# Kernel tuning notes

Measured on AMD Instinct MI355X. Metric: run time of the kernel, lower is better.

## Reference

```python
import jax, jax.numpy as jnp
import numpy as np

VOCAB = 29
VEC = 512      # vector_dim
HID = 1024     # hidden_size
SEN = 64       # sen_len (== seq length)
BATCH = 2048


def setup_inputs() -> dict:
    key = jax.random.key(0)
    k1, k2, k3, k4, k5, k6 = jax.random.split(key, 6)
    s_emb = 1.0
    s_ih = 1.0 / np.sqrt(HID)
    s_cls = 1.0 / np.sqrt(HID)
    return {
        "x": jax.random.randint(k1, (BATCH, SEN), 0, VOCAB, dtype=jnp.int64),
        "emb": jax.random.normal(k2, (VOCAB, VEC), dtype=jnp.float32) * s_emb,
        "W_ih": jax.random.uniform(k3, (HID, VEC), dtype=jnp.float32, minval=-s_ih, maxval=s_ih),
        "W_hh": jax.random.uniform(k4, (HID, HID), dtype=jnp.float32, minval=-s_ih, maxval=s_ih),
        "W_cls": jax.random.uniform(k5, (SEN + 1, HID), dtype=jnp.float32, minval=-s_cls, maxval=s_cls),
        "b_cls": jax.random.uniform(k6, (SEN + 1,), dtype=jnp.float32, minval=-s_cls, maxval=s_cls),
    }


def reference(x, emb, W_ih, W_hh, W_cls, b_cls):
    # Embedding lookup: [B, S, VEC]
    xe = emb[x]
    # Precompute input projections for all timesteps: [B, S, HID]
    xin = jnp.einsum("bsv,hv->bsh", xe, W_ih)

    def step(h, x_t):
        # h: [B, HID], x_t: [B, HID] (already W_ih @ x)
        h_new = jnp.tanh(x_t + h @ W_hh.T)
        return h_new, None

    h0 = jnp.zeros((x.shape[0], HID), dtype=xin.dtype)
    h_last, _ = jax.lax.scan(step, h0, jnp.swapaxes(xin, 0, 1))  # scan over S

    # h.squeeze() in torch (num_layers=1) -> [B, HID]
    logits = h_last @ W_cls.T + b_cls  # [B, SEN+1]
    return logits
```

## Files before the change

### kernel.cpp

```cpp
#include <hip/hip_runtime.h>
#include <hip/hip_bf16.h>

#define VOCAB 29
#define VEC   512
#define HID   1024
#define SEN   64
#define BATCH 2048

typedef __bf16 bf16_t;
typedef bf16_t bf16x8 __attribute__((ext_vector_type(8)));
typedef float  floatx4 __attribute__((ext_vector_type(4)));

__global__ void cvt_whh(const float* __restrict__ w, bf16_t* __restrict__ o, int n) {
    int i = blockIdx.x * blockDim.x + threadIdx.x;
    if (i < n) o[i] = (bf16_t)w[i];
}

__global__ void cvt_wcls(const float* __restrict__ w, bf16_t* __restrict__ o) {
    int i = blockIdx.x * blockDim.x + threadIdx.x;
    if (i >= 80 * HID) return;
    o[i] = (i < 65 * HID) ? (bf16_t)w[i] : (bf16_t)0.0f;
}

__global__ void proj_kernel(const float* __restrict__ emb, const float* __restrict__ wih,
                            float* __restrict__ proj) {
    int idx = blockIdx.x * blockDim.x + threadIdx.x;
    if (idx >= VOCAB * HID) return;
    int v = idx / HID, h = idx % HID;
    const float* e = emb + v * VEC;
    const float* w = wih + h * VEC;
    float s = 0.f;
    for (int k = 0; k < VEC; k += 4) {
        float4 ev = *(const float4*)(e + k);
        float4 wv = *(const float4*)(w + k);
        s += ev.x * wv.x + ev.y * wv.y + ev.z * wv.z + ev.w * wv.w;
    }
    proj[idx] = s;
}

__device__ __forceinline__ float fast_tanh(float x) {
    float e = __expf(2.0f * x);
    return 1.0f - 2.0f / (e + 1.0f);
}

__device__ __forceinline__ void load16_to_lds(const bf16_t* g, bf16_t* l) {
    auto gp = reinterpret_cast<const __attribute__((address_space(1))) unsigned int*>(
        reinterpret_cast<uintptr_t>(g));
    auto lp = reinterpret_cast<__attribute__((address_space(3))) unsigned int*>(
        static_cast<unsigned int>(reinterpret_cast<uintptr_t>(l)));
    __builtin_amdgcn_global_load_lds(gp, lp, 16, 0, 0);
}

#define BM 128
#define BN 64
#define PANEL_BLKS 16
#define SB() __builtin_amdgcn_sched_barrier(0)

#define LOAD_G(B, G) {                                               \
    const int c0_ = 2 * (G);                                         \
    afb[B][0] = *(const bf16x8*)(hA + c0_ * 32);                     \
    afb[B][1] = *(const bf16x8*)(hA + (c0_ + 1) * 32); }

#define COMP_G(B, G)                                                 \
    _Pragma("unroll")                                                \
    for (int j = 0; j < 2; j++) {                                    \
        const int c_ = 2 * (G) + j;                                  \
        const int p_ = ((4 * c_ + q) ^ l7) * 8;                      \
        bf16x8 b0 = *(const bf16x8*)&Bsh[l16][p_];                   \
        bf16x8 b1 = *(const bf16x8*)&Bsh[16 + l16][p_];              \
        bf16x8 b2 = *(const bf16x8*)&Bsh[32 + l16][p_];              \
        bf16x8 b3 = *(const bf16x8*)&Bsh[48 + l16][p_];              \
        bf16x8 a0 = afb[B][j];                                       \
        acc[0] = __builtin_amdgcn_mfma_f32_16x16x32_bf16(a0, b0, acc[0], 0, 0, 0); \
        acc[1] = __builtin_amdgcn_mfma_f32_16x16x32_bf16(a0, b1, acc[1], 0, 0, 0); \
        acc[2] = __builtin_amdgcn_mfma_f32_16x16x32_bf16(a0, b2, acc[2], 0, 0, 0); \
        acc[3] = __builtin_amdgcn_mfma_f32_16x16x32_bf16(a0, b3, acc[3], 0, 0, 0); \
    }

__global__ __launch_bounds__(512, 2)
void rnn_persist(const bf16_t* __restrict__ whh, const float* __restrict__ proj,
                 const int* __restrict__ x, bf16_t* hbuf, int* scnt)
{
    __shared__ __align__(16) bf16_t Bsh[BN][HID];
    __shared__ int uni_sh;

    const int tid  = threadIdx.x;
    const int bx   = blockIdx.x, by = blockIdx.y;
    const int m0   = bx * BM;
    const int n0   = by * BN;
    const int wave = tid >> 6;
    const int lane = tid & 63;
    const int wm   = wave * 16;
    const int q    = lane >> 4;
    const int l16  = lane & 15;
    const int l7   = l16 & 7;

    int* cnt   = scnt + bx * 64;
    int* xmask = scnt + (16 + bx) * 64;

#pragma unroll
    for (int half = 0; half < 2; half++)
#pragma unroll
        for (int it = 0; it < 8; it++) {
            const int r = it * 8 + wave;
            load16_to_lds(whh + (n0 + r) * HID + half * 512 + (lane ^ (r & 7)) * 8,
                          &Bsh[r][half * 512 + lane * 8]);
        }

    int rowl[4];
#pragma unroll
    for (int r = 0; r < 4; r++) rowl[r] = m0 + wm + q * 4 + r;

    {
        float pv0[4][4];
#pragma unroll
        for (int i = 0; i < 4; i++) {
            const int tok = x[rowl[i] * SEN + 0];
            const float* pr = proj + tok * HID + n0;
#pragma unroll
            for (int ni = 0; ni < 4; ni++) pv0[i][ni] = pr[ni * 16 + l16];
        }
#pragma unroll
        for (int i = 0; i < 4; i++)
#pragma unroll
            for (int ni = 0; ni < 4; ni++)
                hbuf[rowl[i] * HID + n0 + ni * 16 + l16] = (bf16_t)fast_tanh(pv0[i][ni]);
    }

    int tk[4];
#pragma unroll
    for (int i = 0; i < 4; i++) tk[i] = x[rowl[i] * SEN + 1];

    __syncthreads();
    if (tid == 0) {
        const int my_xcd = (int)__builtin_amdgcn_s_getreg((3 << 11) | 20);
        __hip_atomic_fetch_or(xmask, 1 << my_xcd, __ATOMIC_RELAXED, __HIP_MEMORY_SCOPE_AGENT);
        __hip_atomic_fetch_add(cnt, 1, __ATOMIC_RELEASE, __HIP_MEMORY_SCOPE_AGENT);
        while (__hip_atomic_load(cnt, __ATOMIC_ACQUIRE, __HIP_MEMORY_SCOPE_AGENT) < PANEL_BLKS)
            __builtin_amdgcn_s_sleep(1);
        const int m = __hip_atomic_load(xmask, __ATOMIC_RELAXED, __HIP_MEMORY_SCOPE_AGENT);
        uni_sh = ((m & (m - 1)) == 0);
    }
    __syncthreads();
    asm volatile("buffer_inv" ::: "memory");
    const int fast = uni_sh;

#pragma unroll 1
    for (int t = 1; t < SEN; t++) {
        const bf16_t* h_in  = hbuf + (size_t)((t + 1) & 1) * (BATCH * HID);
        bf16_t*       h_out = hbuf + (size_t)(t & 1) * (BATCH * HID);

        floatx4 acc[4];
#pragma unroll
        for (int j = 0; j < 4; j++) acc[j] = (floatx4){0.f, 0.f, 0.f, 0.f};

        const bf16_t* hA = h_in + (m0 + wm + l16) * HID + q * 8;
        bf16x8 afb[4][2];

        LOAD_G(0, 0) LOAD_G(1, 1) LOAD_G(2, 2) LOAD_G(3, 3)

        float pv[4][4];
#pragma unroll
        for (int i = 0; i < 4; i++) {
            const float* pr = proj + tk[i] * HID + n0;
#pragma unroll
            for (int ni = 0; ni < 4; ni++) pv[i][ni] = pr[ni * 16 + l16];
        }
        SB();

#pragma unroll
        for (int i = 0; i < 16; i++) {
            COMP_G(i & 3, i)
            if (i < 12) { LOAD_G(i & 3, i + 4) }
            if (i == 12 && t < SEN - 1) {
#pragma unroll
                for (int ii = 0; ii < 4; ii++) tk[ii] = x[rowl[ii] * SEN + t + 1];
            }
            SB();
        }

#pragma unroll
        for (int r = 0; r < 4; r++)
#pragma unroll
            for (int ni = 0; ni < 4; ni++) {
                float v = acc[ni][r] + pv[r][ni];
                h_out[rowl[r] * HID + n0 + ni * 16 + l16] = (bf16_t)fast_tanh(v);
            }

        if (t < SEN - 1) {
            __syncthreads();
            if (fast) {
                if (tid == 0) {
                    __hip_atomic_fetch_add(cnt, 1, __ATOMIC_RELAXED, __HIP_MEMORY_SCOPE_AGENT);
                    while (__hip_atomic_load(cnt, __ATOMIC_RELAXED, __HIP_MEMORY_SCOPE_AGENT)
                           < PANEL_BLKS * (t + 1))
                        __builtin_amdgcn_s_sleep(1);
                }
            } else {
                if (tid == 0) {
                    __hip_atomic_fetch_add(cnt, 1, __ATOMIC_RELEASE, __HIP_MEMORY_SCOPE_AGENT);
                    while (__hip_atomic_load(cnt, __ATOMIC_ACQUIRE, __HIP_MEMORY_SCOPE_AGENT)
                           < PANEL_BLKS * (t + 1))
                        __builtin_amdgcn_s_sleep(1);
                }
            }
            __syncthreads();
            asm volatile("buffer_inv" ::: "memory");
        }
    }
}

#undef LOAD_G
#undef COMP_G

#define CBM 128
#define CLDK 72
__global__ __launch_bounds__(256)
void classifier_mfma(const bf16_t* __restrict__ h, const bf16_t* __restrict__ wcls,
                     const float* __restrict__ bcls, float* __restrict__ out)
{
    __shared__ __align__(16) bf16_t Ash[CBM][CLDK];
    __shared__ __align__(16) bf16_t Bsh[80][CLDK];

    const int tid = threadIdx.x;
    const int m0 = blockIdx.x * CBM;
    const int wave = tid >> 6, lane = tid & 63;
    const int wm = wave * 32;
    const int q = lane >> 4, l16 = lane & 15;

    floatx4 acc[2][5];
#pragma unroll
    for (int i = 0; i < 2; i++)
#pragma unroll
        for (int j = 0; j < 5; j++) acc[i][j] = (floatx4){0.f, 0.f, 0.f, 0.f};

    for (int kk = 0; kk < HID; kk += 64) {
#pragma unroll
        for (int it = 0; it < 4; it++) {
            int idx = tid + it * 256, r = idx >> 3, c = (idx & 7) * 8;
            *(uint4*)&Ash[r][c] = *(const uint4*)&h[(m0 + r) * HID + kk + c];
        }
#pragma unroll
        for (int it = 0; it < 3; it++) {
            int idx = tid + it * 256;
            if (idx < 640) {
                int r = idx >> 3, c = (idx & 7) * 8;
                *(uint4*)&Bsh[r][c] = *(const uint4*)&wcls[r * HID + kk + c];
            }
        }
        __syncthreads();
#pragma unroll
        for (int ks = 0; ks < 64; ks += 32) {
            bf16x8 af[2], bfr[5];
#pragma unroll
            for (int mi = 0; mi < 2; mi++)
                af[mi] = *(const bf16x8*)&Ash[wm + mi * 16 + l16][ks + q * 8];
#pragma unroll
            for (int ni = 0; ni < 5; ni++)
                bfr[ni] = *(const bf16x8*)&Bsh[ni * 16 + l16][ks + q * 8];
#pragma unroll
            for (int mi = 0; mi < 2; mi++)
#pragma unroll
                for (int ni = 0; ni < 5; ni++)
                    acc[mi][ni] = __builtin_amdgcn_mfma_f32_16x16x32_bf16(
                        af[mi], bfr[ni], acc[mi][ni], 0, 0, 0);
        }
        __syncthreads();
    }

#pragma unroll
    for (int mi = 0; mi < 2; mi++) {
#pragma unroll
        for (int r = 0; r < 4; r++) {
            int gm = m0 + wm + mi * 16 + q * 4 + r;
#pragma unroll
            for (int ni = 0; ni < 5; ni++) {
                int gn = ni * 16 + l16;
                if (gn < SEN + 1)
                    out[gm * (SEN + 1) + gn] = acc[mi][ni][r] + bcls[gn];
            }
        }
    }
}

extern "C" void kernel_launch(void* const* d_in, const int* in_sizes, int n_in,
                              void* d_out, int out_size, void* d_ws, size_t ws_size,
                              hipStream_t stream)
{
    const int*   x     = (const int*)  d_in[0];
    const float* emb   = (const float*)d_in[1];
    const float* w_ih  = (const float*)d_in[2];
    const float* w_hh  = (const float*)d_in[3];
    const float* w_cls = (const float*)d_in[4];
    const float* b_cls = (const float*)d_in[5];
    float* out = (float*)d_out;

    char* ws = (char*)d_ws;
    bf16_t* whh_bf  = (bf16_t*)ws;
    float*  proj    = (float*)(ws + (2u << 20));
    bf16_t* wcls_bf = (bf16_t*)(ws + (2u << 20) + (128u << 10));
    bf16_t* h0      = (bf16_t*)(ws + (2u << 20) + (288u << 10));
    bf16_t* h1      = (bf16_t*)(ws + (6u << 20) + (288u << 10));
    int*    scnt    = (int*)   (ws + (10u << 20) + (288u << 10));

    hipMemsetAsync(scnt, 0, 16384, stream);
    cvt_whh<<<(HID * HID) / 256, 256, 0, stream>>>(w_hh, whh_bf, HID * HID);
    proj_kernel<<<(VOCAB * HID + 255) / 256, 256, 0, stream>>>(emb, w_ih, proj);
    cvt_wcls<<<(80 * HID) / 256, 256, 0, stream>>>(w_cls, wcls_bf);

    dim3 grid(BATCH / BM, HID / BN);
    rnn_persist<<<grid, 512, 0, stream>>>(whh_bf, proj, x, h0, scnt);

    classifier_mfma<<<BATCH / CBM, 256, 0, stream>>>(h1, wcls_bf, b_cls, out);
}
```

Measured before the change: 709.8 us.

## Keep W_hh tile in registers and remap waves to a 2x4 MFMA tile grid

The persistent RNN kernel no longer stages its 64x1024 W_hh slice in LDS. Each wave now keeps its 16-column slice of W_hh resident in 32 bf16x8 registers and computes a 64x16 output tile with a 3-deep rotating prefetch of h fragments. This removes the per-step LDS reads of B and changes the wave layout to 2 M-positions by 4 N-positions. In exchange it uses many VGPRs, with possible spilling under launch_bounds(512,2), and each wave reloads A rows that other waves also read. A 96KB dummy shared array is kept, apparently to hold occupancy at the previous level.

Result: slower. 2.405 ms (+238.9%).

```diff
diff --git a/kernel.cpp b/kernel.cpp
--- a/kernel.cpp
+++ b/kernel.cpp
@@ -43,46 +43,16 @@
     return 1.0f - 2.0f / (e + 1.0f);
 }
 
-__device__ __forceinline__ void load16_to_lds(const bf16_t* g, bf16_t* l) {
-    auto gp = reinterpret_cast<const __attribute__((address_space(1))) unsigned int*>(
-        reinterpret_cast<uintptr_t>(g));
-    auto lp = reinterpret_cast<__attribute__((address_space(3))) unsigned int*>(
-        static_cast<unsigned int>(reinterpret_cast<uintptr_t>(l)));
-    __builtin_amdgcn_global_load_lds(gp, lp, 16, 0, 0);
-}
-
 #define BM 128
 #define BN 64
 #define PANEL_BLKS 16
 #define SB() __builtin_amdgcn_sched_barrier(0)
 
-#define LOAD_G(B, G) {                                               \
-    const int c0_ = 2 * (G);                                         \
-    afb[B][0] = *(const bf16x8*)(hA + c0_ * 32);                     \
-    afb[B][1] = *(const bf16x8*)(hA + (c0_ + 1) * 32); }
-
-#define COMP_G(B, G)                                                 \
-    _Pragma("unroll")                                                \
-    for (int j = 0; j < 2; j++) {                                    \
-        const int c_ = 2 * (G) + j;                                  \
-        const int p_ = ((4 * c_ + q) ^ l7) * 8;                      \
-        bf16x8 b0 = *(const bf16x8*)&Bsh[l16][p_];                   \
-        bf16x8 b1 = *(const bf16x8*)&Bsh[16 + l16][p_];              \
-        bf16x8 b2 = *(const bf16x8*)&Bsh[32 + l16][p_];              \
-        bf16x8 b3 = *(const bf16x8*)&Bsh[48 + l16][p_];              \
-        bf16x8 a0 = afb[B][j];                                       \
-        acc[0] = __builtin_amdgcn_mfma_f32_16x16x32_bf16(a0, b0, acc[0], 0, 0, 0); \
-        acc[1] = __builtin_amdgcn_mfma_f32_16x16x32_bf16(a0, b1, acc[1], 0, 0, 0); \
-        acc[2] = __builtin_amdgcn_mfma_f32_16x16x32_bf16(a0, b2, acc[2], 0, 0, 0); \
-        acc[3] = __builtin_amdgcn_mfma_f32_16x16x32_bf16(a0, b3, acc[3], 0, 0, 0); \
-    }
-
 __global__ __launch_bounds__(512, 2)
 void rnn_persist(const bf16_t* __restrict__ whh, const float* __restrict__ proj,
                  const int* __restrict__ x, bf16_t* hbuf, int* scnt)
 {
-    __shared__ __align__(16) bf16_t Bsh[BN][HID];
-    __shared__ int uni_sh;
+    __shared__ int pad[24576];
 
     const int tid  = threadIdx.x;
     const int bx   = blockIdx.x, by = blockIdx.y;
@@ -90,46 +60,31 @@
     const int n0   = by * BN;
     const int wave = tid >> 6;
     const int lane = tid & 63;
-    const int wm   = wave * 16;
     const int q    = lane >> 4;
     const int l16  = lane & 15;
-    const int l7   = l16 & 7;
+    const int npos = wave >> 1;
+    const int mpos = wave & 1;
+
+    const int n_col   = n0 + npos * 16 + l16;
+    const int rowbase = m0 + mpos * 64 + q * 4;
 
     int* cnt   = scnt + bx * 64;
     int* xmask = scnt + (16 + bx) * 64;
 
-#pragma unroll
-    for (int half = 0; half < 2; half++)
-#pragma unroll
-        for (int it = 0; it < 8; it++) {
-            const int r = it * 8 + wave;
-            load16_to_lds(whh + (n0 + r) * HID + half * 512 + (lane ^ (r & 7)) * 8,
-                          &Bsh[r][half * 512 + lane * 8]);
-        }
-
-    int rowl[4];
-#pragma unroll
-    for (int r = 0; r < 4; r++) rowl[r] = m0 + wm + q * 4 + r;
-
+    bf16x8 breg[32];
     {
-        float pv0[4][4];
-#pragma unroll
-        for (int i = 0; i < 4; i++) {
-            const int tok = x[rowl[i] * SEN + 0];
-            const float* pr = proj + tok * HID + n0;
-#pragma unroll
-            for (int ni = 0; ni < 4; ni++) pv0[i][ni] = pr[ni * 16 + l16];
-        }
-#pragma unroll
-        for (int i = 0; i < 4; i++)
-#pragma unroll
-            for (int ni = 0; ni < 4; ni++)
-                hbuf[rowl[i] * HID + n0 + ni * 16 + l16] = (bf16_t)fast_tanh(pv0[i][ni]);
-    }
-
-    int tk[4];
-#pragma unroll
-    for (int i = 0; i < 4; i++) tk[i] = x[rowl[i] * SEN + 1];
+        const bf16_t* wB = whh + (size_t)n_col * HID + q * 8;
+#pragma unroll
+        for (int c = 0; c < 32; c++) breg[c] = *(const bf16x8*)(wB + c * 32);
+    }
+
+#pragma unroll
+    for (int i = 0; i < 16; i++) {
+        const int row = rowbase + (i >> 2) * 16 + (i & 3);
+        const int tok = x[row * SEN + 0];
+        const float v = proj[tok * HID + n_col];
+        hbuf[row * HID + n_col] = (bf16_t)fast_tanh(v);
+    }
 
     __syncthreads();
     if (tid == 0) {
@@ -139,11 +94,11 @@
         while (__hip_atomic_load(cnt, __ATOMIC_ACQUIRE, __HIP_MEMORY_SCOPE_AGENT) < PANEL_BLKS)
             __builtin_amdgcn_s_sleep(1);
         const int m = __hip_atomic_load(xmask, __ATOMIC_RELAXED, __HIP_MEMORY_SCOPE_AGENT);
-        uni_sh = ((m & (m - 1)) == 0);
+        pad[0] = ((m & (m - 1)) == 0);
     }
     __syncthreads();
     asm volatile("buffer_inv" ::: "memory");
-    const int fast = uni_sh;
+    const int fast = pad[0];
 
 #pragma unroll 1
     for (int t = 1; t < SEN; t++) {
@@ -154,38 +109,47 @@
 #pragma unroll
         for (int j = 0; j < 4; j++) acc[j] = (floatx4){0.f, 0.f, 0.f, 0.f};
 
-        const bf16_t* hA = h_in + (m0 + wm + l16) * HID + q * 8;
-        bf16x8 afb[4][2];
-
-        LOAD_G(0, 0) LOAD_G(1, 1) LOAD_G(2, 2) LOAD_G(3, 3)
-
-        float pv[4][4];
-#pragma unroll
-        for (int i = 0; i < 4; i++) {
-            const float* pr = proj + tk[i] * HID + n0;
-#pragma unroll
-            for (int ni = 0; ni < 4; ni++) pv[i][ni] = pr[ni * 16 + l16];
-        }
+        const bf16_t* hA[4];
+#pragma unroll
+        for (int mf = 0; mf < 4; mf++)
+            hA[mf] = h_in + (size_t)(m0 + mpos * 64 + mf * 16 + l16) * HID + q * 8;
+
+        bf16x8 afr[3][4];
+        int tk[16];
+
+#pragma unroll
+        for (int d = 0; d < 3; d++)
+#pragma unroll
+            for (int mf = 0; mf < 4; mf++)
+                afr[d][mf] = *(const bf16x8*)(hA[mf] + d * 32);
         SB();
 
 #pragma unroll
+        for (int c = 0; c < 32; c++) {
+            const int slot = c % 3;
+#pragma unroll
+            for (int mf = 0; mf < 4; mf++)
+                acc[mf] = __builtin_amdgcn_mfma_f32_16x16x32_bf16(
+                    afr[slot][mf], breg[c], acc[mf], 0, 0, 0);
+            if (c < 29) {
+#pragma unroll
+                for (int mf = 0; mf < 4; mf++)
+                    afr[slot][mf] = *(const bf16x8*)(hA[mf] + (c + 3) * 32);
+            }
+            if (c == 16) {
+#pragma unroll
+                for (int i = 0; i < 16; i++)
+                    tk[i] = x[(rowbase + (i >> 2) * 16 + (i & 3)) * SEN + t];
+            }
+            SB();
+        }
+
+#pragma unroll
         for (int i = 0; i < 16; i++) {
-            COMP_G(i & 3, i)
-            if (i < 12) { LOAD_G(i & 3, i + 4) }
-            if (i == 12 && t < SEN - 1) {
-#pragma unroll
-                for (int ii = 0; ii < 4; ii++) tk[ii] = x[rowl[ii] * SEN + t + 1];
-            }
-            SB();
-        }
-
-#pragma unroll
-        for (int r = 0; r < 4; r++)
-#pragma unroll
-            for (int ni = 0; ni < 4; ni++) {
-                float v = acc[ni][r] + pv[r][ni];
-                h_out[rowl[r] * HID + n0 + ni * 16 + l16] = (bf16_t)fast_tanh(v);
-            }
+            const int row = rowbase + (i >> 2) * 16 + (i & 3);
+            const float v = acc[i >> 2][i & 3] + proj[tk[i] * HID + n_col];
+            h_out[row * HID + n_col] = (bf16_t)fast_tanh(v);
+        }
 
         if (t < SEN - 1) {
             __syncthreads();
@@ -210,9 +174,6 @@
     }
 }
 
-#undef LOAD_G
-#undef COMP_G
-
 #define CBM 128
 #define CLDK 72
 __global__ __launch_bounds__(256)
```

## Reshape per-wave MFMA tile to 32x32 in the persistent RNN step

Applied to the files above, without the earlier changes.

Each of the 8 waves now computes a 32-row by 32-column tile (2x2 MFMA fragments) instead of 16 rows by the full 64 columns. Every A fragment loaded from global memory is reused across two column fragments and every B fragment from LDS across two row fragments. This halves the LDS B reads per MFMA and changes the global h reads from 16 rows per wave to 32, so each row is now fetched by two waves. The A prefetch ring grows to 8 slots with two fragments each, which raises register pressure under launch_bounds(512,2).

Result: slower. 1.135 ms (+60.0%).

```diff
diff --git a/kernel.cpp b/kernel.cpp
--- a/kernel.cpp
+++ b/kernel.cpp
@@ -56,27 +56,6 @@
 #define PANEL_BLKS 16
 #define SB() __builtin_amdgcn_sched_barrier(0)
 
-#define LOAD_G(B, G) {                                               \
-    const int c0_ = 2 * (G);                                         \
-    afb[B][0] = *(const bf16x8*)(hA + c0_ * 32);                     \
-    afb[B][1] = *(const bf16x8*)(hA + (c0_ + 1) * 32); }
-
-#define COMP_G(B, G)                                                 \
-    _Pragma("unroll")                                                \
-    for (int j = 0; j < 2; j++) {                                    \
-        const int c_ = 2 * (G) + j;                                  \
-        const int p_ = ((4 * c_ + q) ^ l7) * 8;                      \
-        bf16x8 b0 = *(const bf16x8*)&Bsh[l16][p_];                   \
-        bf16x8 b1 = *(const bf16x8*)&Bsh[16 + l16][p_];              \
-        bf16x8 b2 = *(const bf16x8*)&Bsh[32 + l16][p_];              \
-        bf16x8 b3 = *(const bf16x8*)&Bsh[48 + l16][p_];              \
-        bf16x8 a0 = afb[B][j];                                       \
-        acc[0] = __builtin_amdgcn_mfma_f32_16x16x32_bf16(a0, b0, acc[0], 0, 0, 0); \
-        acc[1] = __builtin_amdgcn_mfma_f32_16x16x32_bf16(a0, b1, acc[1], 0, 0, 0); \
-        acc[2] = __builtin_amdgcn_mfma_f32_16x16x32_bf16(a0, b2, acc[2], 0, 0, 0); \
-        acc[3] = __builtin_amdgcn_mfma_f32_16x16x32_bf16(a0, b3, acc[3], 0, 0, 0); \
-    }
-
 __global__ __launch_bounds__(512, 2)
 void rnn_persist(const bf16_t* __restrict__ whh, const float* __restrict__ proj,
                  const int* __restrict__ x, bf16_t* hbuf, int* scnt)
@@ -90,10 +69,11 @@
     const int n0   = by * BN;
     const int wave = tid >> 6;
     const int lane = tid & 63;
-    const int wm   = wave * 16;
     const int q    = lane >> 4;
     const int l16  = lane & 15;
     const int l7   = l16 & 7;
+    const int mpos = wave & 3;
+    const int npos = wave >> 2;
 
     int* cnt   = scnt + bx * 64;
     int* xmask = scnt + (16 + bx) * 64;
@@ -107,29 +87,29 @@
                           &Bsh[r][half * 512 + lane * 8]);
         }
 
-    int rowl[4];
-#pragma unroll
-    for (int r = 0; r < 4; r++) rowl[r] = m0 + wm + q * 4 + r;
+    int rowl[8];
+#pragma unroll
+    for (int mf = 0; mf < 2; mf++)
+#pragma unroll
+        for (int r = 0; r < 4; r++)
+            rowl[mf * 4 + r] = m0 + mpos * 32 + mf * 16 + q * 4 + r;
+    const int ncol0 = n0 + npos * 32 + l16;
 
     {
-        float pv0[4][4];
-#pragma unroll
-        for (int i = 0; i < 4; i++) {
+#pragma unroll
+        for (int i = 0; i < 8; i++) {
             const int tok = x[rowl[i] * SEN + 0];
-            const float* pr = proj + tok * HID + n0;
-#pragma unroll
-            for (int ni = 0; ni < 4; ni++) pv0[i][ni] = pr[ni * 16 + l16];
-        }
-#pragma unroll
-        for (int i = 0; i < 4; i++)
-#pragma unroll
-            for (int ni = 0; ni < 4; ni++)
-                hbuf[rowl[i] * HID + n0 + ni * 16 + l16] = (bf16_t)fast_tanh(pv0[i][ni]);
-    }
-
-    int tk[4];
-#pragma unroll
-    for (int i = 0; i < 4; i++) tk[i] = x[rowl[i] * SEN + 1];
+#pragma unroll
+            for (int ni = 0; ni < 2; ni++) {
+                const float v = proj[tok * HID + ncol0 + ni * 16];
+                hbuf[rowl[i] * HID + ncol0 + ni * 16] = (bf16_t)fast_tanh(v);
+            }
+        }
+    }
+
+    int tk[8];
+#pragma unroll
+    for (int i = 0; i < 8; i++) tk[i] = x[rowl[i] * SEN + 1];
 
     __syncthreads();
     if (tid == 0) {
@@ -150,42 +130,62 @@
         const bf16_t* h_in  = hbuf + (size_t)((t + 1) & 1) * (BATCH * HID);
         bf16_t*       h_out = hbuf + (size_t)(t & 1) * (BATCH * HID);
 
-        floatx4 acc[4];
-#pragma unroll
-        for (int j = 0; j < 4; j++) acc[j] = (floatx4){0.f, 0.f, 0.f, 0.f};
-
-        const bf16_t* hA = h_in + (m0 + wm + l16) * HID + q * 8;
-        bf16x8 afb[4][2];
-
-        LOAD_G(0, 0) LOAD_G(1, 1) LOAD_G(2, 2) LOAD_G(3, 3)
-
-        float pv[4][4];
-#pragma unroll
-        for (int i = 0; i < 4; i++) {
-            const float* pr = proj + tk[i] * HID + n0;
-#pragma unroll
-            for (int ni = 0; ni < 4; ni++) pv[i][ni] = pr[ni * 16 + l16];
+        floatx4 acc[2][2];
+#pragma unroll
+        for (int i = 0; i < 2; i++)
+#pragma unroll
+            for (int j = 0; j < 2; j++) acc[i][j] = (floatx4){0.f, 0.f, 0.f, 0.f};
+
+        const bf16_t* hA = h_in + (size_t)(m0 + mpos * 32 + l16) * HID + q * 8;
+
+        bf16x8 afr[8][2];
+
+#pragma unroll
+        for (int d = 0; d < 8; d++) {
+            afr[d][0] = *(const bf16x8*)(hA + d * 32);
+            afr[d][1] = *(const bf16x8*)(hA + 16 * HID + d * 32);
+        }
+
+        float pv[8][2];
+#pragma unroll
+        for (int i = 0; i < 8; i++) {
+            const float* pr = proj + tk[i] * HID + ncol0;
+            pv[i][0] = pr[0];
+            pv[i][1] = pr[16];
         }
         SB();
 
 #pragma unroll
-        for (int i = 0; i < 16; i++) {
-            COMP_G(i & 3, i)
-            if (i < 12) { LOAD_G(i & 3, i + 4) }
-            if (i == 12 && t < SEN - 1) {
-#pragma unroll
-                for (int ii = 0; ii < 4; ii++) tk[ii] = x[rowl[ii] * SEN + t + 1];
+        for (int c = 0; c < 32; c++) {
+            const int slot = c & 7;
+            const int pq = ((4 * c + q) ^ l7) * 8;
+            bf16x8 b0 = *(const bf16x8*)&Bsh[npos * 32 + l16][pq];
+            bf16x8 b1 = *(const bf16x8*)&Bsh[npos * 32 + 16 + l16][pq];
+            acc[0][0] = __builtin_amdgcn_mfma_f32_16x16x32_bf16(afr[slot][0], b0, acc[0][0], 0, 0, 0);
+            acc[0][1] = __builtin_amdgcn_mfma_f32_16x16x32_bf16(afr[slot][0], b1, acc[0][1], 0, 0, 0);
+            acc[1][0] = __builtin_amdgcn_mfma_f32_16x16x32_bf16(afr[slot][1], b0, acc[1][0], 0, 0, 0);
+            acc[1][1] = __builtin_amdgcn_mfma_f32_16x16x32_bf16(afr[slot][1], b1, acc[1][1], 0, 0, 0);
+            if (c < 24) {
+                afr[slot][0] = *(const bf16x8*)(hA + (c + 8) * 32);
+                afr[slot][1] = *(const bf16x8*)(hA + 16 * HID + (c + 8) * 32);
+            }
+            if (c == 24 && t < SEN - 1) {
+#pragma unroll
+                for (int i = 0; i < 8; i++) tk[i] = x[rowl[i] * SEN + t + 1];
             }
             SB();
         }
 
 #pragma unroll
-        for (int r = 0; r < 4; r++)
-#pragma unroll
-            for (int ni = 0; ni < 4; ni++) {
-                float v = acc[ni][r] + pv[r][ni];
-                h_out[rowl[r] * HID + n0 + ni * 16 + l16] = (bf16_t)fast_tanh(v);
-            }
+        for (int mf = 0; mf < 2; mf++)
+#pragma unroll
+            for (int r = 0; r < 4; r++)
+#pragma unroll
+                for (int ni = 0; ni < 2; ni++) {
+                    const int i = mf * 4 + r;
+                    const float v = acc[mf][ni][r] + pv[i][ni];
+                    h_out[rowl[i] * HID + ncol0 + ni * 16] = (bf16_t)fast_tanh(v);
+                }
 
         if (t < SEN - 1) {
             __syncthreads();
@@ -210,9 +210,6 @@
     }
 }
 
-#undef LOAD_G
-#undef COMP_G
-
 #define CBM 128
 #define CLDK 72
 __global__ __launch_bounds__(256)
```
